# Performance work log

Measured on AMD Instinct MI355X. Metric: run time of the kernel, lower is better.

## Reference

```python
import jax, jax.numpy as jnp
import numpy as np

STATE, DESIRES, H = 256, 128, 512  # hidden chain: [512, 512, 512] (last = action_size)
B, N_LAYERS = 512, 2


def setup_inputs() -> dict:
    key = jax.random.key(0)
    ks = jax.random.split(key, 10)
    s = lambda k, shape, fan_in: jax.random.normal(k, shape, jnp.float32) / np.sqrt(fan_in)
    return {
        "state": jax.random.normal(ks[0], (B, STATE), jnp.float32),
        "command": jax.random.normal(ks[1], (B, DESIRES), jnp.float32),
        "embed_w": s(ks[2], (STATE, H), STATE),
        "embed_b": jnp.zeros((H,), jnp.float32),
        # stacked hypernet params for the 2 identical-shape layers
        "hw_W": s(ks[3], (N_LAYERS, DESIRES, H * H), DESIRES),
        "hw_b": s(ks[4], (N_LAYERS, H * H), DESIRES),
        "hb_W": s(ks[5], (N_LAYERS, DESIRES, H), DESIRES),
        "hb_b": s(ks[6], (N_LAYERS, H), DESIRES),
    }


def reference(state, command, embed_w, embed_b, hw_W, hw_b, hb_W, hb_b):
    # embed: Linear + Tanh  -> [B, H]
    out = jnp.tanh(state @ embed_w + embed_b)
    for i in range(N_LAYERS):
        # per-sample weight matrix [B, H, H] generated from command
        w = (command @ hw_W[i] + hw_b[i]).reshape(-1, H, H)
        b = command @ hb_W[i] + hb_b[i]  # [B, H]
        # batched 1xH vec-matmul + bias + ReLU (ReLU applied on ALL layers, as in source)
        out = jax.nn.relu(jnp.einsum("bh,bho->bo", out, w) + b)
    return out
```

## Files before the change

kernel.cpp:

```cpp
#include <hip/hip_runtime.h>
#include <hip/hip_bf16.h>


typedef __bf16 bf16x8 __attribute__((ext_vector_type(8)));
typedef float  f32x4  __attribute__((ext_vector_type(4)));

#define LDS_PITCH 72

__global__ __launch_bounds__(512) void embed_kernel(
    const float* __restrict__ state,
    const float* __restrict__ ew,
    const float* __restrict__ eb,
    __bf16* __restrict__ act0)
{
    const int o  = threadIdx.x;
    const int r0 = blockIdx.x * 4;
    float bias = eb[o];
    float acc[4] = {bias, bias, bias, bias};
    for (int s = 0; s < 256; ++s) {
        float wv = ew[s * 512 + o];
        #pragma unroll
        for (int r = 0; r < 4; ++r)
            acc[r] = fmaf(state[(r0 + r) * 256 + s], wv, acc[r]);
    }
    #pragma unroll
    for (int r = 0; r < 4; ++r)
        act0[(r0 + r) * 512 + o] = (__bf16)tanhf(acc[r]);
}

__global__ __launch_bounds__(512, 2) void hyper_gemm(
    const float* __restrict__ Wl,
    const float* __restrict__ hwbl,
    const float* __restrict__ cmd,
    const __bf16* __restrict__ act,
    float* __restrict__ partial)
{
    __shared__ __bf16 lds[2][64][LDS_PITCH];

    const int nt   = blockIdx.x;
    const int g    = blockIdx.y;
    const int n0   = nt * 64;
    const int tid  = threadIdx.x;
    const int lane = tid & 63;
    const int wv   = tid >> 6;
    const int l15  = lane & 15;
    const int lg   = lane >> 4;
    const int m_base = wv * 64;

    const int sr = tid >> 4;
    const int so = (tid & 15) * 4;

    const int nit = 32 + (g < 8 ? 1 : 0);

    f32x4 Yacc[4][4];
    f32x4 Gacc[4][4];
    #pragma unroll
    for (int a = 0; a < 4; ++a)
        #pragma unroll
        for (int b = 0; b < 4; ++b) { Yacc[a][b] = (f32x4)0.f; Gacc[a][b] = (f32x4)0.f; }

    {
        const float* p = Wl + (size_t)(g << 2) * 262144 + n0;
        f32x4 va = *(const f32x4*)(p + sr * 512 + so);
        f32x4 vb = *(const f32x4*)(p + (sr + 32) * 512 + so);
        #pragma unroll
        for (int q = 0; q < 4; ++q) {
            lds[0][so + q][sr]      = (__bf16)va[q];
            lds[0][so + q][sr + 32] = (__bf16)vb[q];
        }
    }
    __syncthreads();

    int cur = 0;
    for (int i = 0; i < nit; ++i) {
        const bool hn = (i + 1 < nit);
        f32x4 na, nb;
        if (hn) {
            const int j = i + 1;
            const float* p;
            if (j < 32) {
                int d  = (g << 2) + (j >> 3);
                int h0 = (j & 7) << 6;
                p = Wl + (size_t)d * 262144 + (size_t)h0 * 512 + n0;
            } else {
                p = hwbl + (size_t)(g << 6) * 512 + n0;
            }
            na = *(const f32x4*)(p + sr * 512 + so);
            nb = *(const f32x4*)(p + (sr + 32) * 512 + so);
        }

        const int h0 = (i < 32) ? ((i & 7) << 6) : (g << 6);

        #pragma unroll
        for (int kk = 0; kk < 2; ++kk) {
            bf16x8 afr[4], bfr[4];
            #pragma unroll
            for (int mi = 0; mi < 4; ++mi)
                afr[mi] = *(const bf16x8*)(act + (m_base + mi * 16 + l15) * 512
                                               + h0 + kk * 32 + lg * 8);
            #pragma unroll
            for (int ni = 0; ni < 4; ++ni)
                bfr[ni] = *(const bf16x8*)(&lds[cur][ni * 16 + l15][kk * 32 + lg * 8]);
            #pragma unroll
            for (int mi = 0; mi < 4; ++mi)
                #pragma unroll
                for (int ni = 0; ni < 4; ++ni)
                    Gacc[mi][ni] = __builtin_amdgcn_mfma_f32_16x16x32_bf16(
                        afr[mi], bfr[ni], Gacc[mi][ni], 0, 0, 0);
        }

        if (i < 32) {
            if ((i & 7) == 7) {
                const int d = (g << 2) + (i >> 3);
                #pragma unroll
                for (int mi = 0; mi < 4; ++mi) {
                    float cv[4];
                    #pragma unroll
                    for (int r = 0; r < 4; ++r)
                        cv[r] = cmd[(m_base + mi * 16 + lg * 4 + r) * 128 + d];
                    #pragma unroll
                    for (int ni = 0; ni < 4; ++ni)
                        #pragma unroll
                        for (int r = 0; r < 4; ++r) {
                            Yacc[mi][ni][r] = fmaf(cv[r], Gacc[mi][ni][r], Yacc[mi][ni][r]);
                            Gacc[mi][ni][r] = 0.f;
                        }
                }
            }
        } else {
            #pragma unroll
            for (int mi = 0; mi < 4; ++mi)
                #pragma unroll
                for (int ni = 0; ni < 4; ++ni)
                    #pragma unroll
                    for (int r = 0; r < 4; ++r) {
                        Yacc[mi][ni][r] += Gacc[mi][ni][r];
                        Gacc[mi][ni][r] = 0.f;
                    }
        }

        __syncthreads();
        if (hn) {
            #pragma unroll
            for (int q = 0; q < 4; ++q) {
                lds[cur ^ 1][so + q][sr]      = (__bf16)na[q];
                lds[cur ^ 1][so + q][sr + 32] = (__bf16)nb[q];
            }
        }
        __syncthreads();
        cur ^= 1;
    }

    float* pp = partial + (size_t)g * 262144 + n0;
    #pragma unroll
    for (int mi = 0; mi < 4; ++mi)
        #pragma unroll
        for (int r = 0; r < 4; ++r) {
            int m = m_base + mi * 16 + lg * 4 + r;
            #pragma unroll
            for (int ni = 0; ni < 4; ++ni)
                pp[m * 512 + ni * 16 + l15] = Yacc[mi][ni][r];
        }
}

__global__ __launch_bounds__(512) void epilogue_kernel(
    const float* __restrict__ partial,
    const float* __restrict__ cmd,
    const float* __restrict__ hbWl,
    const float* __restrict__ hbbl,
    __bf16* __restrict__ act_out,
    float* __restrict__ final_out)
{
    const int o  = threadIdx.x;
    const int r0 = blockIdx.x * 2;
    float a0 = hbbl[o];
    float a1 = a0;
    for (int d = 0; d < 128; ++d) {
        float wv = hbWl[d * 512 + o];
        a0 = fmaf(cmd[r0 * 128 + d],       wv, a0);
        a1 = fmaf(cmd[(r0 + 1) * 128 + d], wv, a1);
    }
    for (int s = 0; s < 32; ++s) {
        a0 += partial[((size_t)s * 512 + r0)     * 512 + o];
        a1 += partial[((size_t)s * 512 + r0 + 1) * 512 + o];
    }
    a0 = fmaxf(a0, 0.f);
    a1 = fmaxf(a1, 0.f);
    if (act_out) {
        act_out[r0 * 512 + o]       = (__bf16)a0;
        act_out[(r0 + 1) * 512 + o] = (__bf16)a1;
    } else {
        final_out[r0 * 512 + o]       = a0;
        final_out[(r0 + 1) * 512 + o] = a1;
    }
}

extern "C" void kernel_launch(void* const* d_in, const int* in_sizes, int n_in,
                              void* d_out, int out_size, void* d_ws, size_t ws_size,
                              hipStream_t stream) {
    const float* state = (const float*)d_in[0];
    const float* cmd   = (const float*)d_in[1];
    const float* ew    = (const float*)d_in[2];
    const float* eb    = (const float*)d_in[3];
    const float* hwW   = (const float*)d_in[4];
    const float* hwb   = (const float*)d_in[5];
    const float* hbW   = (const float*)d_in[6];
    const float* hbb   = (const float*)d_in[7];
    float* out = (float*)d_out;

    char* ws = (char*)d_ws;
    __bf16* act0   = (__bf16*)ws;
    __bf16* act1   = (__bf16*)(ws + 512 * 1024);
    float*  partial = (float*)(ws + 1024 * 1024);

    embed_kernel<<<128, 512, 0, stream>>>(state, ew, eb, act0);

    hyper_gemm<<<dim3(8, 32), 512, 0, stream>>>(
        hwW, hwb, cmd, act0, partial);
    epilogue_kernel<<<256, 512, 0, stream>>>(
        partial, cmd, hbW, hbb, act1, nullptr);

    hyper_gemm<<<dim3(8, 32), 512, 0, stream>>>(
        hwW + (size_t)128 * 262144, hwb + 262144, cmd, act1, partial);
    epilogue_kernel<<<256, 512, 0, stream>>>(
        partial, cmd, hbW + 128 * 512, hbb + 512, nullptr, out);
}
```

Measured before the change: 549.6 us.

## Halve hyper-GEMM N tile, deepen prefetch to two stages, single sync per iteration

The hyper_gemm tile width drops from 64 to 32 columns, which doubles the grid to 16x32 blocks and raises the occupancy hint to 4 blocks per CU. The global-to-LDS staging now prefetches two tiles ahead and needs one barrier per iteration instead of two. The embed and epilogue kernels each process fewer rows per block so more blocks launch, and the epilogue splits the partial-sum reduction across four accumulators. The aim is to fill more CUs and hide the fp32 weight streaming latency. The cost is that each block re-reads the activation A fragments for half as many output columns, which doubles A traffic.

```diff
diff --git a/kernel.cpp b/kernel.cpp
--- a/kernel.cpp
+++ b/kernel.cpp
@@ -5,7 +5,7 @@
 typedef __bf16 bf16x8 __attribute__((ext_vector_type(8)));
 typedef float  f32x4  __attribute__((ext_vector_type(4)));
 
-#define LDS_PITCH 72
+#define PITCH 72
 
 __global__ __launch_bounds__(512) void embed_kernel(
     const float* __restrict__ state,
@@ -14,32 +14,30 @@
     __bf16* __restrict__ act0)
 {
     const int o  = threadIdx.x;
-    const int r0 = blockIdx.x * 4;
-    float bias = eb[o];
-    float acc[4] = {bias, bias, bias, bias};
+    const int r0 = blockIdx.x * 2;
+    float b  = eb[o];
+    float a0 = b, a1 = b;
     for (int s = 0; s < 256; ++s) {
         float wv = ew[s * 512 + o];
-        #pragma unroll
-        for (int r = 0; r < 4; ++r)
-            acc[r] = fmaf(state[(r0 + r) * 256 + s], wv, acc[r]);
+        a0 = fmaf(state[r0 * 256 + s],       wv, a0);
+        a1 = fmaf(state[(r0 + 1) * 256 + s], wv, a1);
     }
-    #pragma unroll
-    for (int r = 0; r < 4; ++r)
-        act0[(r0 + r) * 512 + o] = (__bf16)tanhf(acc[r]);
+    act0[r0 * 512 + o]       = (__bf16)tanhf(a0);
+    act0[(r0 + 1) * 512 + o] = (__bf16)tanhf(a1);
 }
 
-__global__ __launch_bounds__(512, 2) void hyper_gemm(
+__global__ __launch_bounds__(512, 4) void hyper_gemm(
     const float* __restrict__ Wl,
     const float* __restrict__ hwbl,
     const float* __restrict__ cmd,
     const __bf16* __restrict__ act,
     float* __restrict__ partial)
 {
-    __shared__ __bf16 lds[2][64][LDS_PITCH];
+    __shared__ __bf16 lds[2][32][PITCH];
 
     const int nt   = blockIdx.x;
     const int g    = blockIdx.y;
-    const int n0   = nt * 64;
+    const int n0   = nt * 32;
     const int tid  = threadIdx.x;
     const int lane = tid & 63;
     const int wv   = tid >> 6;
@@ -47,66 +45,55 @@
     const int lg   = lane >> 4;
     const int m_base = wv * 64;
 
-    const int sr = tid >> 4;
-    const int so = (tid & 15) * 4;
+    const int so = (tid & 7) * 4;
+    const int sh = tid >> 3;
 
     const int nit = 32 + (g < 8 ? 1 : 0);
 
-    f32x4 Yacc[4][4];
-    f32x4 Gacc[4][4];
+    f32x4 Y[4][2], G[4][2];
     #pragma unroll
     for (int a = 0; a < 4; ++a)
         #pragma unroll
-        for (int b = 0; b < 4; ++b) { Yacc[a][b] = (f32x4)0.f; Gacc[a][b] = (f32x4)0.f; }
+        for (int b = 0; b < 2; ++b) { Y[a][b] = (f32x4)0.f; G[a][b] = (f32x4)0.f; }
 
-    {
-        const float* p = Wl + (size_t)(g << 2) * 262144 + n0;
-        f32x4 va = *(const f32x4*)(p + sr * 512 + so);
-        f32x4 vb = *(const f32x4*)(p + (sr + 32) * 512 + so);
-        #pragma unroll
-        for (int q = 0; q < 4; ++q) {
-            lds[0][so + q][sr]      = (__bf16)va[q];
-            lds[0][so + q][sr + 32] = (__bf16)vb[q];
-        }
-    }
-    __syncthreads();
+    #define TILE_PTR(j) ((j) < 32 \
+        ? Wl + (size_t)((g << 2) + ((j) >> 3)) * 262144 + (size_t)(((j) & 7) << 6) * 512 + n0 \
+        : hwbl + (size_t)(g << 6) * 512 + n0)
+
+    f32x4 na = *(const f32x4*)(TILE_PTR(0) + sh * 512 + so);
+    #pragma unroll
+    for (int q = 0; q < 4; ++q) lds[0][so + q][sh] = (__bf16)na[q];
+    na = *(const f32x4*)(TILE_PTR(1) + sh * 512 + so);
 
     int cur = 0;
     for (int i = 0; i < nit; ++i) {
-        const bool hn = (i + 1 < nit);
-        f32x4 na, nb;
-        if (hn) {
-            const int j = i + 1;
-            const float* p;
-            if (j < 32) {
-                int d  = (g << 2) + (j >> 3);
-                int h0 = (j & 7) << 6;
-                p = Wl + (size_t)d * 262144 + (size_t)h0 * 512 + n0;
-            } else {
-                p = hwbl + (size_t)(g << 6) * 512 + n0;
-            }
-            na = *(const f32x4*)(p + sr * 512 + so);
-            nb = *(const f32x4*)(p + (sr + 32) * 512 + so);
+        __syncthreads();
+
+        if (i + 1 < nit) {
+            #pragma unroll
+            for (int q = 0; q < 4; ++q) lds[cur ^ 1][so + q][sh] = (__bf16)na[q];
         }
+        if (i + 2 < nit)
+            na = *(const f32x4*)(TILE_PTR(i + 2) + sh * 512 + so);
 
         const int h0 = (i < 32) ? ((i & 7) << 6) : (g << 6);
 
         #pragma unroll
         for (int kk = 0; kk < 2; ++kk) {
-            bf16x8 afr[4], bfr[4];
+            bf16x8 afr[4], bfr[2];
             #pragma unroll
             for (int mi = 0; mi < 4; ++mi)
                 afr[mi] = *(const bf16x8*)(act + (m_base + mi * 16 + l15) * 512
                                                + h0 + kk * 32 + lg * 8);
             #pragma unroll
-            for (int ni = 0; ni < 4; ++ni)
+            for (int ni = 0; ni < 2; ++ni)
                 bfr[ni] = *(const bf16x8*)(&lds[cur][ni * 16 + l15][kk * 32 + lg * 8]);
             #pragma unroll
             for (int mi = 0; mi < 4; ++mi)
                 #pragma unroll
-                for (int ni = 0; ni < 4; ++ni)
-                    Gacc[mi][ni] = __builtin_amdgcn_mfma_f32_16x16x32_bf16(
-                        afr[mi], bfr[ni], Gacc[mi][ni], 0, 0, 0);
+                for (int ni = 0; ni < 2; ++ni)
+                    G[mi][ni] = __builtin_amdgcn_mfma_f32_16x16x32_bf16(
+                        afr[mi], bfr[ni], G[mi][ni], 0, 0, 0);
         }
 
         if (i < 32) {
@@ -114,42 +101,29 @@
                 const int d = (g << 2) + (i >> 3);
                 #pragma unroll
                 for (int mi = 0; mi < 4; ++mi) {
-                    float cv[4];
                     #pragma unroll
-                    for (int r = 0; r < 4; ++r)
-                        cv[r] = cmd[(m_base + mi * 16 + lg * 4 + r) * 128 + d];
-                    #pragma unroll
-                    for (int ni = 0; ni < 4; ++ni)
+                    for (int r = 0; r < 4; ++r) {
+                        float cvv = cmd[(m_base + mi * 16 + lg * 4 + r) * 128 + d];
                         #pragma unroll
-                        for (int r = 0; r < 4; ++r) {
-                            Yacc[mi][ni][r] = fmaf(cv[r], Gacc[mi][ni][r], Yacc[mi][ni][r]);
-                            Gacc[mi][ni][r] = 0.f;
+                        for (int ni = 0; ni < 2; ++ni) {
+                            Y[mi][ni][r] = fmaf(cvv, G[mi][ni][r], Y[mi][ni][r]);
+                            G[mi][ni][r] = 0.f;
                         }
+                    }
                 }
             }
         } else {
             #pragma unroll
             for (int mi = 0; mi < 4; ++mi)
                 #pragma unroll
-                for (int ni = 0; ni < 4; ++ni)
+                for (int ni = 0; ni < 2; ++ni)
                     #pragma unroll
-                    for (int r = 0; r < 4; ++r) {
-                        Yacc[mi][ni][r] += Gacc[mi][ni][r];
-                        Gacc[mi][ni][r] = 0.f;
-                    }
+                    for (int r = 0; r < 4; ++r)
+                        Y[mi][ni][r] += G[mi][ni][r];
         }
-
-        __syncthreads();
-        if (hn) {
-            #pragma unroll
-            for (int q = 0; q < 4; ++q) {
-                lds[cur ^ 1][so + q][sr]      = (__bf16)na[q];
-                lds[cur ^ 1][so + q][sr + 32] = (__bf16)nb[q];
-            }
-        }
-        __syncthreads();
         cur ^= 1;
     }
+    #undef TILE_PTR
 
     float* pp = partial + (size_t)g * 262144 + n0;
     #pragma unroll
@@ -158,8 +132,8 @@
         for (int r = 0; r < 4; ++r) {
             int m = m_base + mi * 16 + lg * 4 + r;
             #pragma unroll
-            for (int ni = 0; ni < 4; ++ni)
-                pp[m * 512 + ni * 16 + l15] = Yacc[mi][ni][r];
+            for (int ni = 0; ni < 2; ++ni)
+                pp[m * 512 + ni * 16 + l15] = Y[mi][ni][r];
         }
 }
 
@@ -171,28 +145,22 @@
     __bf16* __restrict__ act_out,
     float* __restrict__ final_out)
 {
-    const int o  = threadIdx.x;
-    const int r0 = blockIdx.x * 2;
-    float a0 = hbbl[o];
-    float a1 = a0;
-    for (int d = 0; d < 128; ++d) {
-        float wv = hbWl[d * 512 + o];
-        a0 = fmaf(cmd[r0 * 128 + d],       wv, a0);
-        a1 = fmaf(cmd[(r0 + 1) * 128 + d], wv, a1);
+    const int o = threadIdx.x;
+    const int r = blockIdx.x;
+    float a = hbbl[o];
+    for (int d = 0; d < 128; ++d)
+        a = fmaf(cmd[r * 128 + d], hbWl[d * 512 + o], a);
+    float s0 = 0.f, s1 = 0.f, s2 = 0.f, s3 = 0.f;
+    #pragma unroll
+    for (int gq = 0; gq < 32; gq += 4) {
+        s0 += partial[((size_t)(gq + 0) * 512 + r) * 512 + o];
+        s1 += partial[((size_t)(gq + 1) * 512 + r) * 512 + o];
+        s2 += partial[((size_t)(gq + 2) * 512 + r) * 512 + o];
+        s3 += partial[((size_t)(gq + 3) * 512 + r) * 512 + o];
     }
-    for (int s = 0; s < 32; ++s) {
-        a0 += partial[((size_t)s * 512 + r0)     * 512 + o];
-        a1 += partial[((size_t)s * 512 + r0 + 1) * 512 + o];
-    }
-    a0 = fmaxf(a0, 0.f);
-    a1 = fmaxf(a1, 0.f);
-    if (act_out) {
-        act_out[r0 * 512 + o]       = (__bf16)a0;
-        act_out[(r0 + 1) * 512 + o] = (__bf16)a1;
-    } else {
-        final_out[r0 * 512 + o]       = a0;
-        final_out[(r0 + 1) * 512 + o] = a1;
-    }
+    a = fmaxf(a + (s0 + s1) + (s2 + s3), 0.f);
+    if (act_out) act_out[r * 512 + o] = (__bf16)a;
+    else         final_out[r * 512 + o] = a;
 }
 
 extern "C" void kernel_launch(void* const* d_in, const int* in_sizes, int n_in,
@@ -209,19 +177,17 @@
     float* out = (float*)d_out;
 
     char* ws = (char*)d_ws;
-    __bf16* act0   = (__bf16*)ws;
-    __bf16* act1   = (__bf16*)(ws + 512 * 1024);
+    __bf16* act0    = (__bf16*)ws;
+    __bf16* act1    = (__bf16*)(ws + 512 * 1024);
     float*  partial = (float*)(ws + 1024 * 1024);
 
-    embed_kernel<<<128, 512, 0, stream>>>(state, ew, eb, act0);
+    embed_kernel<<<256, 512, 0, stream>>>(state, ew, eb, act0);
 
-    hyper_gemm<<<dim3(8, 32), 512, 0, stream>>>(
-        hwW, hwb, cmd, act0, partial);
-    epilogue_kernel<<<256, 512, 0, stream>>>(
-        partial, cmd, hbW, hbb, act1, nullptr);
+    hyper_gemm<<<dim3(16, 32), 512, 0, stream>>>(hwW, hwb, cmd, act0, partial);
+    epilogue_kernel<<<512, 512, 0, stream>>>(partial, cmd, hbW, hbb, act1, nullptr);
 
-    hyper_gemm<<<dim3(8, 32), 512, 0, stream>>>(
+    hyper_gemm<<<dim3(16, 32), 512, 0, stream>>>(
         hwW + (size_t)128 * 262144, hwb + 262144, cmd, act1, partial);
-    epilogue_kernel<<<256, 512, 0, stream>>>(
+    epilogue_kernel<<<512, 512, 0, stream>>>(
         partial, cmd, hbW + 128 * 512, hbb + 512, nullptr, out);
 }
```

After: 638.6 us. +16.2%, slower.
